# Performance work log

Hardware: AMD Instinct MI355X
Metric: run time of the kernel (lower is better)

The kernel has to match this reference:

```python
import jax, jax.numpy as jnp
import numpy as np

B, S, HID = 2, 2048, 1024
H = 16
D = HID // H  # 64
SCALE = 1.0 / float(np.sqrt(D))


def setup_inputs() -> dict:
    key = jax.random.key(0)
    ks = jax.random.split(key, 12)
    s = 0.02
    return {
        "query": jax.random.normal(ks[0], (B, S, HID), jnp.float32),
        "key": jax.random.normal(ks[1], (B, S, HID), jnp.float32),
        "value": jax.random.normal(ks[2], (B, S, HID), jnp.float32),
        "attention_mask": jnp.ones((B, S, S), jnp.int32),
        "Wq": jax.random.normal(ks[3], (HID, HID), jnp.float32) * s,
        "bq": jnp.zeros((HID,), jnp.float32),
        "Wk": jax.random.normal(ks[4], (HID, HID), jnp.float32) * s,
        "bk": jnp.zeros((HID,), jnp.float32),
        "Wv": jax.random.normal(ks[5], (HID, HID), jnp.float32) * s,
        "bv": jnp.zeros((HID,), jnp.float32),
        "Wo": jax.random.normal(ks[6], (HID, HID), jnp.float32) * s,
        "bo": jnp.zeros((HID,), jnp.float32),
    }


def _split_heads(x):  # [B,S,HID] -> [B,H,S,D]
    b, s, _ = x.shape
    return x.reshape(b, s, H, D).transpose(0, 2, 1, 3)


def reference(query, key, value, attention_mask, Wq, bq, Wk, bk, Wv, bv, Wo, bo):
    # Projections (torch Linear: x @ W.T + b)
    Q = _split_heads(query @ Wq.T + bq)
    K = _split_heads(key @ Wk.T + bk)
    V = _split_heads(value @ Wv.T + bv)
    # Full attention; chunking in the original is math-equivalent (softmax over full key axis per chunk)
    scores = jnp.einsum("bhqd,bhkd->bhqk", Q, K) * SCALE
    scores = jnp.where(attention_mask[:, None, :, :] == 0, jnp.float32(-1e9), scores)
    attn = jax.nn.softmax(scores, axis=-1)  # dropout is identity in eval mode
    ctx = jnp.einsum("bhqk,bhkd->bhqd", attn, V)
    ctx = ctx.transpose(0, 2, 1, 3).reshape(query.shape[0], query.shape[1], HID)
    out = ctx @ Wo.T + bo
    # module returns a dummy uniform attention-weight tensor
    attn_weights = jnp.full((query.shape[0], H, S, S), 1.0 / S, dtype=query.dtype)
    return (out, attn_weights)
```

## Files before the change

kernel.cpp:

```cpp
#include <hip/hip_runtime.h>

typedef float f4v __attribute__((ext_vector_type(4)));
typedef short s4v __attribute__((ext_vector_type(4)));
typedef short s8v __attribute__((ext_vector_type(8)));
typedef __bf16 bf8v __attribute__((ext_vector_type(8)));
typedef unsigned short u16;
typedef unsigned int u32;

#define S_LEN 2048
#define HIDN 1024
#define NH 16
#define HD 64
#define SC2 0.180336879f
#define DTH 11.5415603f
#define FILLV 0.00048828125f

__device__ __forceinline__ u16 f2bf(float f) {
  unsigned u = __builtin_bit_cast(unsigned, f);
  u = u + 0x7FFFu + ((u >> 16) & 1u);
  return (u16)(u >> 16);
}

__device__ __forceinline__ f4v mfma16(s8v a, s8v b, f4v c) {
  return __builtin_amdgcn_mfma_f32_16x16x32_bf16(
      __builtin_bit_cast(bf8v, a), __builtin_bit_cast(bf8v, b), c, 0, 0, 0);
}

__device__ __forceinline__ void gl16(const void* g, void* l) {
  __builtin_amdgcn_global_load_lds((const __attribute__((address_space(1))) u32*)g,
                                   (__attribute__((address_space(3))) u32*)l, 16, 0, 0);
}

__device__ __forceinline__ s8v cvt8(f4v x, f4v y) {
  s8v r;
  r[0] = (short)f2bf(x[0]); r[1] = (short)f2bf(x[1]);
  r[2] = (short)f2bf(x[2]); r[3] = (short)f2bf(x[3]);
  r[4] = (short)f2bf(y[0]); r[5] = (short)f2bf(y[1]);
  r[6] = (short)f2bf(y[2]); r[7] = (short)f2bf(y[3]);
  return r;
}

#define FILL_DECL(nblk)                                        \
  const f4v fvv = (f4v){FILLV, FILLV, FILLV, FILLV};           \
  f4v* fp = fillb + (size_t)bid * 256 + threadIdx.x;           \
  f4v* const fpe = fillb + fill4;                               \
  const size_t FT = (size_t)(nblk) * 256;

#define FILL_STORE()                                           \
  do { if (fp < fpe) __builtin_nontemporal_store(fvv, fp);     \
       fp += FT; } while (0)

struct CvtWArgs { const float* s[4]; u16* d[4]; };

__global__ __launch_bounds__(256) void cvt_w(CvtWArgs a, unsigned* flg) {
  if (blockIdx.x == 0 && blockIdx.y == 0 && threadIdx.x == 0) flg[0] = 1u;
  const float* s = a.s[blockIdx.y];
  u16* d = a.d[blockIdx.y];
  const int stride = gridDim.x * 256;
  for (int i = blockIdx.x * 256 + threadIdx.x; i < 131072; i += stride) {
    const f4v x0 = ((const f4v*)s)[2 * i];
    const f4v x1 = ((const f4v*)s)[2 * i + 1];
    ((s8v*)d)[i] = cvt8(x0, x1);
  }
}

__global__ void pack_mask(const int* __restrict__ mask, unsigned* __restrict__ pmo,
                          unsigned* __restrict__ flg) {
  const size_t total = (size_t)2 * S_LEN * S_LEN;
  size_t i = (size_t)blockIdx.x * blockDim.x + threadIdx.x;
  const size_t st = (size_t)gridDim.x * blockDim.x;
  const int lane = threadIdx.x & 63;
  for (; i < total; i += st) {
    const unsigned long long bb = __ballot(mask[i] != 0);
    if (lane == 0) pmo[i >> 5] = (unsigned)bb;
    if (lane == 32) pmo[i >> 5] = (unsigned)(bb >> 32);
    if (lane == 0 && bb != ~0ull) flg[0] = 0u;
  }
}

struct QkvArgs {
  const float* A[3]; const u16* W[3]; const float* bias[3]; u16* out[3];
  f4v* fillb; size_t fill4;
};

__global__ __launch_bounds__(256) void gemm_qkv(QkvArgs ga) {
  __shared__ __align__(16) u16 As[128 * 32];
  __shared__ __align__(16) u16 Bs[128 * 32];
  const int p = blockIdx.x;
  const int xcd = p & 7;
  const int ii = p >> 3;
  const int ytile = xcd * 12 + (ii >> 3);
  const int xt = ii & 7;
  const int id = ytile >> 5;
  const int tid = threadIdx.x;
  const int lane = tid & 63;
  const int wv = tid >> 6;
  const int wm = wv >> 1, wn = wv & 1;
  const int g = lane >> 4, l15 = lane & 15;
  const int m0 = (ytile & 31) * 128, n0 = xt * 128;
  const int bid = p;
  f4v* fillb = ga.fillb;
  const size_t fill4 = ga.fill4;
  FILL_DECL(768);

  f4v acc[4][4];
#pragma unroll
  for (int i = 0; i < 4; ++i)
#pragma unroll
    for (int j = 0; j < 4; ++j) acc[i][j] = (f4v){0.f, 0.f, 0.f, 0.f};

  const int ar = tid >> 1;
  const int ac = (tid & 1) * 16;
  const float* ap = ga.A[id] + (size_t)(m0 + ar) * HIDN + ac;
  const u16* bp0 = ga.W[id] + (size_t)(n0 + (tid >> 2)) * HIDN + (tid & 3) * 8;
  const u16* bp1 = bp0 + (size_t)64 * HIDN;
  u16* bsl0 = Bs + tid * 8;
  u16* bsl1 = Bs + 2048 + tid * 8;
  u16* asl = As + ar * 32 + ac;

  for (int kt = 0; kt < HIDN; kt += 32) {
    const f4v a0 = ((const f4v*)(ap + kt))[0];
    const f4v a1 = ((const f4v*)(ap + kt))[1];
    const f4v a2 = ((const f4v*)(ap + kt))[2];
    const f4v a3 = ((const f4v*)(ap + kt))[3];
    __syncthreads();
    gl16(bp0 + kt, bsl0);
    gl16(bp1 + kt, bsl1);
    *(s8v*)asl = cvt8(a0, a1);
    *(s8v*)(asl + 8) = cvt8(a2, a3);
    FILL_STORE();
    FILL_STORE();
    __syncthreads();
    s8v af[4], bfv[4];
#pragma unroll
    for (int i = 0; i < 4; ++i)
      af[i] = *(const s8v*)(As + (wm * 64 + i * 16 + l15) * 32 + g * 8);
#pragma unroll
    for (int j = 0; j < 4; ++j)
      bfv[j] = *(const s8v*)(Bs + (wn * 64 + j * 16 + l15) * 32 + g * 8);
#pragma unroll
    for (int i = 0; i < 4; ++i)
#pragma unroll
      for (int j = 0; j < 4; ++j) acc[i][j] = mfma16(af[i], bfv[j], acc[i][j]);
  }

  const float* bias = ga.bias[id];
  u16* out = ga.out[id];
  const int mode2 = (id == 2);
#pragma unroll
  for (int i = 0; i < 4; ++i) {
#pragma unroll
    for (int j = 0; j < 4; ++j) {
      const int mb = m0 + wm * 64 + i * 16 + g * 4;
      const int n = n0 + wn * 64 + j * 16 + l15;
      const float bv = bias[n];
#pragma unroll
      for (int r = 0; r < 4; ++r) {
        const int m = mb + r;
        const float v = acc[i][j][r] + bv;
        const int b = m >> 11, s = m & 2047, h = n >> 6, d = n & 63;
        if (mode2) {
          out[((size_t)(b * NH + h) * HD + d) * S_LEN + s] = f2bf(v);
        } else {
          out[(((size_t)(b * NH + h) * S_LEN + s) << 6) + d] = f2bf(v);
        }
      }
    }
  }
}

__global__ __launch_bounds__(256) void attn_fused(
    const u16* __restrict__ Qb, const u16* __restrict__ Kb,
    const u16* __restrict__ Vtb, u16* __restrict__ ctxb,
    const unsigned* __restrict__ pm, const unsigned* __restrict__ flg,
    f4v* __restrict__ fillb, const size_t fill4) {
  __shared__ __align__(16) u16 Ks[64 * 64];
  __shared__ __align__(16) u16 Vs[64 * 64];
  __shared__ __align__(16) u16 Ps[4][2][16 * 64];
  __shared__ unsigned mw[128][2];

  const int p = blockIdx.x;
  const int xcd = p & 7;
  const int ii = p >> 3;
  const int bh = xcd * 4 + (ii >> 4);
  const int q0 = (ii & 15) * 128;
  const int tid = threadIdx.x;
  const int lane = tid & 63;
  const int wv = tid >> 6;
  const int g = lane >> 4, l15 = lane & 15;
  const int b = bh >> 4, h = bh & 15;
  const bool allones = (flg[0] != 0u);
  const int bid = p;
  FILL_DECL(512);

  s8v qb[2][2];
#pragma unroll
  for (int qg = 0; qg < 2; ++qg) {
    const u16* qp = Qb + ((size_t)bh * S_LEN + q0 + wv * 32 + qg * 16 + l15) * HD + g * 8;
    qb[qg][0] = *(const s8v*)qp;
    qb[qg][1] = *(const s8v*)(qp + 32);
  }

  f4v o[2][4];
#pragma unroll
  for (int qg = 0; qg < 2; ++qg)
#pragma unroll
    for (int nb = 0; nb < 4; ++nb) o[qg][nb] = (f4v){0.f, 0.f, 0.f, 0.f};
  float mr[2] = {-INFINITY, -INFINITY}, lr[2] = {0.f, 0.f};

  const int sr = tid >> 3;
  const int sg = tid & 7;
  const int sc0 = ((sg ^ (sr & 7)) * 8);
  const u16* kp0 = Kb + ((size_t)bh * S_LEN + sr) * HD + sc0;
  const u16* kp1 = kp0 + (size_t)32 * HD;
  const u16* vp0 = Vtb + ((size_t)bh * HD + sr) * S_LEN + sc0;
  const u16* vp1 = vp0 + (size_t)32 * S_LEN;
  u16* kl = Ks + tid * 8;
  u16* vl = Vs + tid * 8;

  for (int kt = 0; kt < S_LEN; kt += 64) {
    __syncthreads();
    gl16(kp0 + (size_t)kt * HD, kl);
    gl16(kp1 + (size_t)kt * HD, kl + 2048);
    gl16(vp0 + kt, vl);
    gl16(vp1 + kt, vl + 2048);
    if (!allones) {
      mw[tid >> 1][tid & 1] =
          pm[((size_t)b * S_LEN + q0 + (tid >> 1)) * (S_LEN / 32) + (kt >> 5) + (tid & 1)];
    }
    FILL_STORE();
    FILL_STORE();
    FILL_STORE();
    FILL_STORE();
    __syncthreads();

    f4v sc[2][4];
    __builtin_amdgcn_s_setprio(1);
#pragma unroll
    for (int nb = 0; nb < 4; ++nb) {
      const int kr = nb * 16 + l15;
      const s8v ka0 = *(const s8v*)(Ks + kr * 64 + ((g ^ (kr & 7)) * 8));
      const s8v ka1 = *(const s8v*)(Ks + kr * 64 + (((4 + g) ^ (kr & 7)) * 8));
#pragma unroll
      for (int qg = 0; qg < 2; ++qg) {
        f4v z = (f4v){0.f, 0.f, 0.f, 0.f};
        z = mfma16(ka0, qb[qg][0], z);
        z = mfma16(ka1, qb[qg][1], z);
        sc[qg][nb] = z * SC2;
      }
    }
    __builtin_amdgcn_s_setprio(0);
    if (!allones) {
#pragma unroll
      for (int qg = 0; qg < 2; ++qg) {
        const int qr = wv * 32 + qg * 16 + l15;
        const unsigned w0 = mw[qr][0], w1 = mw[qr][1];
#pragma unroll
        for (int nb = 0; nb < 4; ++nb) {
          const unsigned wmk = (nb < 2) ? w0 : w1;
#pragma unroll
          for (int r = 0; r < 4; ++r) {
            const int bit = ((nb & 1) << 4) + (g << 2) + r;
            if (!((wmk >> bit) & 1u)) sc[qg][nb][r] = -1e9f;
          }
        }
      }
    }

#pragma unroll
    for (int qg = 0; qg < 2; ++qg) {
      float tm = sc[qg][0][0];
#pragma unroll
      for (int nb = 0; nb < 4; ++nb)
#pragma unroll
        for (int r = 0; r < 4; ++r) tm = fmaxf(tm, sc[qg][nb][r]);
      tm = fmaxf(tm, __shfl_xor(tm, 16, 64));
      tm = fmaxf(tm, __shfl_xor(tm, 32, 64));
      if (!__all(tm <= mr[qg] + DTH)) {
        const float mn = fmaxf(mr[qg], tm);
        const float al = exp2f(mr[qg] - mn);
        mr[qg] = mn;
        lr[qg] *= al;
#pragma unroll
        for (int r = 0; r < 4; ++r) {
          const float ar = __shfl(al, (g << 2) + r, 64);
#pragma unroll
          for (int nb = 0; nb < 4; ++nb) o[qg][nb][r] *= ar;
        }
      }
      float rs = 0.f;
#pragma unroll
      for (int nb = 0; nb < 4; ++nb)
#pragma unroll
        for (int r = 0; r < 4; ++r) {
          const float p_ = exp2f(sc[qg][nb][r] - mr[qg]);
          sc[qg][nb][r] = p_;
          rs += p_;
        }
      rs += __shfl_xor(rs, 16, 64);
      rs += __shfl_xor(rs, 32, 64);
      lr[qg] += rs;
#pragma unroll
      for (int nb = 0; nb < 4; ++nb) {
        s4v pk;
        pk[0] = (short)f2bf(sc[qg][nb][0]);
        pk[1] = (short)f2bf(sc[qg][nb][1]);
        pk[2] = (short)f2bf(sc[qg][nb][2]);
        pk[3] = (short)f2bf(sc[qg][nb][3]);
        *(s4v*)(Ps[wv][qg] + l15 * 64 + ((nb * 16 + g * 4) ^ ((l15 & 7) * 8))) = pk;
      }
    }

    s8v pa[2][2];
#pragma unroll
    for (int qg = 0; qg < 2; ++qg)
#pragma unroll
      for (int kk = 0; kk < 2; ++kk)
        pa[qg][kk] = *(const s8v*)(Ps[wv][qg] + l15 * 64 + (((kk * 4 + g) ^ (l15 & 7)) * 8));

    __builtin_amdgcn_s_setprio(1);
#pragma unroll
    for (int nb = 0; nb < 4; ++nb) {
      const int vr = nb * 16 + l15;
      const s8v vb0 = *(const s8v*)(Vs + vr * 64 + ((g ^ (vr & 7)) * 8));
      const s8v vb1 = *(const s8v*)(Vs + vr * 64 + (((4 + g) ^ (vr & 7)) * 8));
#pragma unroll
      for (int qg = 0; qg < 2; ++qg) {
        o[qg][nb] = mfma16(pa[qg][0], vb0, o[qg][nb]);
        o[qg][nb] = mfma16(pa[qg][1], vb1, o[qg][nb]);
      }
    }
    __builtin_amdgcn_s_setprio(0);
  }

#pragma unroll
  for (int qg = 0; qg < 2; ++qg)
#pragma unroll
    for (int r = 0; r < 4; ++r) {
      const float linv = 1.f / __shfl(lr[qg], (g << 2) + r, 64);
      const int q = q0 + wv * 32 + qg * 16 + g * 4 + r;
#pragma unroll
      for (int nb = 0; nb < 4; ++nb) {
        const int d = nb * 16 + l15;
        ctxb[(((size_t)b * S_LEN + q) * NH + h) * HD + d] = f2bf(o[qg][nb][r] * linv);
      }
    }
}

__global__ __launch_bounds__(256) void gemm_out(
    const u16* __restrict__ A, const u16* __restrict__ W,
    const float* __restrict__ bias, float* __restrict__ out,
    f4v* __restrict__ fillb, const size_t fill4) {
  __shared__ __align__(16) u16 As[128 * 32];
  __shared__ __align__(16) u16 Bs[64 * 32];
  const int p = blockIdx.x;
  const int xcd = p & 7;
  const int ii = p >> 3;
  const int m0 = (xcd * 4 + (ii >> 4)) * 128;
  const int n0 = (ii & 15) * 64;
  const int tid = threadIdx.x;
  const int lane = tid & 63;
  const int wv = tid >> 6;
  const int wm = wv >> 1, wn = wv & 1;
  const int g = lane >> 4, l15 = lane & 15;
  const int bid = p;
  FILL_DECL(512);

  f4v acc[4][2];
#pragma unroll
  for (int i = 0; i < 4; ++i)
#pragma unroll
    for (int j = 0; j < 2; ++j) acc[i][j] = (f4v){0.f, 0.f, 0.f, 0.f};

  const u16* ap0 = A + (size_t)(m0 + (tid >> 2)) * HIDN + (tid & 3) * 8;
  const u16* ap1 = ap0 + (size_t)64 * HIDN;
  const u16* bp0 = W + (size_t)(n0 + (tid >> 2)) * HIDN + (tid & 3) * 8;
  u16* asl0 = As + tid * 8;
  u16* asl1 = As + 2048 + tid * 8;
  u16* bsl0 = Bs + tid * 8;

  for (int kt = 0; kt < HIDN; kt += 32) {
    __syncthreads();
    gl16(ap0 + kt, asl0);
    gl16(ap1 + kt, asl1);
    gl16(bp0 + kt, bsl0);
    FILL_STORE();
    __syncthreads();
    s8v af[4], bfv[2];
#pragma unroll
    for (int i = 0; i < 4; ++i)
      af[i] = *(const s8v*)(As + (wm * 64 + i * 16 + l15) * 32 + g * 8);
#pragma unroll
    for (int j = 0; j < 2; ++j)
      bfv[j] = *(const s8v*)(Bs + (wn * 32 + j * 16 + l15) * 32 + g * 8);
#pragma unroll
    for (int i = 0; i < 4; ++i)
#pragma unroll
      for (int j = 0; j < 2; ++j) acc[i][j] = mfma16(af[i], bfv[j], acc[i][j]);
  }

#pragma unroll
  for (int i = 0; i < 4; ++i) {
#pragma unroll
    for (int j = 0; j < 2; ++j) {
      const int mb = m0 + wm * 64 + i * 16 + g * 4;
      const int n = n0 + wn * 32 + j * 16 + l15;
      const float bv = bias[n];
#pragma unroll
      for (int r = 0; r < 4; ++r) {
        out[(size_t)(mb + r) * HIDN + n] = acc[i][j][r] + bv;
      }
    }
  }
}

__global__ void fill_tail(float* __restrict__ p, const size_t n4) {
  const f4v v = (f4v){FILLV, FILLV, FILLV, FILLV};
  size_t i = (size_t)blockIdx.x * blockDim.x + threadIdx.x;
  const size_t st = (size_t)gridDim.x * blockDim.x;
  f4v* p4 = (f4v*)p;
  for (; i < n4; i += st) p4[i] = v;
}

extern "C" void kernel_launch(void* const* d_in, const int* in_sizes, int n_in,
                              void* d_out, int out_size, void* d_ws, size_t ws_size,
                              hipStream_t stream) {
  const float* query = (const float*)d_in[0];
  const float* key_ = (const float*)d_in[1];
  const float* value = (const float*)d_in[2];
  const int* amask = (const int*)d_in[3];
  const float* Wq = (const float*)d_in[4];
  const float* bq = (const float*)d_in[5];
  const float* Wk = (const float*)d_in[6];
  const float* bk = (const float*)d_in[7];
  const float* Wv = (const float*)d_in[8];
  const float* bv = (const float*)d_in[9];
  const float* Wo = (const float*)d_in[10];
  const float* bo = (const float*)d_in[11];

  float* out = (float*)d_out;
  const size_t OUT0 = (size_t)2 * S_LEN * HIDN;
  float* outw = out + OUT0;

  const size_t MB = (size_t)1 << 20;
  const size_t CARVE = 48 * MB;
  const bool use_ws = ws_size >= CARVE;
  char* scratch = use_ws ? (char*)d_ws : (char*)outw;

  u16* wq16 = (u16*)(scratch);
  u16* wk16 = (u16*)(scratch + 2 * MB);
  u16* wv16 = (u16*)(scratch + 4 * MB);
  u16* wo16 = (u16*)(scratch + 6 * MB);
  u16* Qb = (u16*)(scratch + 8 * MB);
  u16* Kb = (u16*)(scratch + 16 * MB);
  u16* Vtb = (u16*)(scratch + 24 * MB);
  u16* ctxb = (u16*)(scratch + 32 * MB);
  unsigned* pm = (unsigned*)(scratch + 40 * MB);
  unsigned* flg = (unsigned*)(scratch + 41 * MB);

  f4v* fillp;
  size_t F;
  if (use_ws) {
    fillp = (f4v*)outw;
    F = 33554432;
  } else {
    fillp = (f4v*)(outw + CARVE / 4);
    F = 33554432 - CARVE / 16;
  }
  const size_t capq = (size_t)768 * 256 * 64;
  const size_t capa = (size_t)512 * 256 * 128;
  const size_t cq = F < capq ? F : capq;
  const size_t F1 = F - cq;
  const size_t ca = F1 < capa ? F1 : capa;
  const size_t co = F1 - ca;
  f4v* fq = fillp;
  f4v* fa = fq + cq;
  f4v* fo = fa + ca;

  CvtWArgs cw;
  cw.s[0] = Wq; cw.s[1] = Wk; cw.s[2] = Wv; cw.s[3] = Wo;
  cw.d[0] = wq16; cw.d[1] = wk16; cw.d[2] = wv16; cw.d[3] = wo16;
  cvt_w<<<dim3(64, 4), 256, 0, stream>>>(cw, flg);
  pack_mask<<<1024, 256, 0, stream>>>(amask, pm, flg);

  QkvArgs qa;
  qa.A[0] = query; qa.A[1] = key_; qa.A[2] = value;
  qa.W[0] = wq16; qa.W[1] = wk16; qa.W[2] = wv16;
  qa.bias[0] = bq; qa.bias[1] = bk; qa.bias[2] = bv;
  qa.out[0] = Qb; qa.out[1] = Kb; qa.out[2] = Vtb;
  qa.fillb = fq; qa.fill4 = cq;
  gemm_qkv<<<768, 256, 0, stream>>>(qa);

  attn_fused<<<512, 256, 0, stream>>>(Qb, Kb, Vtb, ctxb, pm, flg, fa, ca);

  gemm_out<<<512, 256, 0, stream>>>(ctxb, wo16, bo, out, fo, co);

  if (!use_ws) {
    fill_tail<<<2048, 256, 0, stream>>>(outw, CARVE / 16);
  }
}
```

Before: 203.6 us.

## Halve attention query tile, merge prep kernels, fold Q scale into projection

The attention kernel now handles 64 queries per block (16 per wave) across 1024 blocks instead of 128 per block across 512, which cuts registers and LDS per block and adds parallelism. It also folds the softmax scale into the Q projection epilogue, swaps manual bf16 rounding for native vector conversions, and merges weight conversion and mask packing into one prep kernel with an inverted flag set by memset. Fill stores are moved after the barrier in the GEMMs. The cost is twice as many K/V tile loads from global memory per head and an extra memset launch.

```diff
diff --git a/kernel.cpp b/kernel.cpp
--- a/kernel.cpp
+++ b/kernel.cpp
@@ -1,9 +1,11 @@
 #include <hip/hip_runtime.h>
 
 typedef float f4v __attribute__((ext_vector_type(4)));
+typedef float f8v __attribute__((ext_vector_type(8)));
 typedef short s4v __attribute__((ext_vector_type(4)));
 typedef short s8v __attribute__((ext_vector_type(8)));
-typedef __bf16 bf8v __attribute__((ext_vector_type(8)));
+typedef __bf16 bf4t __attribute__((ext_vector_type(4)));
+typedef __bf16 bf8t __attribute__((ext_vector_type(8)));
 typedef unsigned short u16;
 typedef unsigned int u32;
 
@@ -11,33 +13,31 @@
 #define HIDN 1024
 #define NH 16
 #define HD 64
-#define SC2 0.180336879f
+#define QS 0.180336879f
 #define DTH 11.5415603f
 #define FILLV 0.00048828125f
 
 __device__ __forceinline__ u16 f2bf(float f) {
-  unsigned u = __builtin_bit_cast(unsigned, f);
-  u = u + 0x7FFFu + ((u >> 16) & 1u);
-  return (u16)(u >> 16);
+  return __builtin_bit_cast(u16, (__bf16)f);
+}
+
+__device__ __forceinline__ s8v cvt8(f4v x, f4v y) {
+  const f8v f = {x[0], x[1], x[2], x[3], y[0], y[1], y[2], y[3]};
+  return __builtin_bit_cast(s8v, __builtin_convertvector(f, bf8t));
+}
+
+__device__ __forceinline__ s4v cvt4(f4v x) {
+  return __builtin_bit_cast(s4v, __builtin_convertvector(x, bf4t));
 }
 
 __device__ __forceinline__ f4v mfma16(s8v a, s8v b, f4v c) {
   return __builtin_amdgcn_mfma_f32_16x16x32_bf16(
-      __builtin_bit_cast(bf8v, a), __builtin_bit_cast(bf8v, b), c, 0, 0, 0);
+      __builtin_bit_cast(bf8t, a), __builtin_bit_cast(bf8t, b), c, 0, 0, 0);
 }
 
 __device__ __forceinline__ void gl16(const void* g, void* l) {
   __builtin_amdgcn_global_load_lds((const __attribute__((address_space(1))) u32*)g,
                                    (__attribute__((address_space(3))) u32*)l, 16, 0, 0);
-}
-
-__device__ __forceinline__ s8v cvt8(f4v x, f4v y) {
-  s8v r;
-  r[0] = (short)f2bf(x[0]); r[1] = (short)f2bf(x[1]);
-  r[2] = (short)f2bf(x[2]); r[3] = (short)f2bf(x[3]);
-  r[4] = (short)f2bf(y[0]); r[5] = (short)f2bf(y[1]);
-  r[6] = (short)f2bf(y[2]); r[7] = (short)f2bf(y[3]);
-  return r;
 }
 
 #define FILL_DECL(nblk)                                        \
@@ -50,31 +50,33 @@
   do { if (fp < fpe) __builtin_nontemporal_store(fvv, fp);     \
        fp += FT; } while (0)
 
-struct CvtWArgs { const float* s[4]; u16* d[4]; };
-
-__global__ __launch_bounds__(256) void cvt_w(CvtWArgs a, unsigned* flg) {
-  if (blockIdx.x == 0 && blockIdx.y == 0 && threadIdx.x == 0) flg[0] = 1u;
-  const float* s = a.s[blockIdx.y];
-  u16* d = a.d[blockIdx.y];
-  const int stride = gridDim.x * 256;
-  for (int i = blockIdx.x * 256 + threadIdx.x; i < 131072; i += stride) {
-    const f4v x0 = ((const f4v*)s)[2 * i];
-    const f4v x1 = ((const f4v*)s)[2 * i + 1];
-    ((s8v*)d)[i] = cvt8(x0, x1);
-  }
-}
-
-__global__ void pack_mask(const int* __restrict__ mask, unsigned* __restrict__ pmo,
-                          unsigned* __restrict__ flg) {
-  const size_t total = (size_t)2 * S_LEN * S_LEN;
-  size_t i = (size_t)blockIdx.x * blockDim.x + threadIdx.x;
-  const size_t st = (size_t)gridDim.x * blockDim.x;
-  const int lane = threadIdx.x & 63;
-  for (; i < total; i += st) {
-    const unsigned long long bb = __ballot(mask[i] != 0);
-    if (lane == 0) pmo[i >> 5] = (unsigned)bb;
-    if (lane == 32) pmo[i >> 5] = (unsigned)(bb >> 32);
-    if (lane == 0 && bb != ~0ull) flg[0] = 0u;
+struct PrepArgs { const float* w[4]; u16* d[4]; const int* mask; unsigned* pm; unsigned* flg; };
+
+__global__ __launch_bounds__(256) void prep(PrepArgs a) {
+  const int y = blockIdx.y;
+  const int tid = threadIdx.x;
+  if (y < 4) {
+    const float* s = a.w[y];
+    u16* d = a.d[y];
+#pragma unroll
+    for (int j = 0; j < 2; ++j) {
+      const int i = blockIdx.x * 256 + tid + j * 65536;
+      const f4v x0 = ((const f4v*)s)[2 * i];
+      const f4v x1 = ((const f4v*)s)[2 * i + 1];
+      ((s8v*)d)[i] = cvt8(x0, x1);
+    }
+  } else {
+    const int lane = tid & 63;
+    const size_t base = (size_t)(y - 4) * 2097152;
+    bool anyz = false;
+    for (int j = 0; j < 32; ++j) {
+      const size_t i = base + (size_t)blockIdx.x * 256 + tid + (size_t)j * 65536;
+      const unsigned long long bb = __ballot(a.mask[i] != 0);
+      if (lane == 0) a.pm[i >> 5] = (unsigned)bb;
+      if (lane == 32) a.pm[i >> 5] = (unsigned)(bb >> 32);
+      anyz |= (bb != ~0ull);
+    }
+    if (anyz && lane == 0) a.flg[0] = 1u;
   }
 }
 
@@ -128,9 +130,9 @@
     gl16(bp1 + kt, bsl1);
     *(s8v*)asl = cvt8(a0, a1);
     *(s8v*)(asl + 8) = cvt8(a2, a3);
+    __syncthreads();
     FILL_STORE();
     FILL_STORE();
-    __syncthreads();
     s8v af[4], bfv[4];
 #pragma unroll
     for (int i = 0; i < 4; ++i)
@@ -147,6 +149,7 @@
   const float* bias = ga.bias[id];
   u16* out = ga.out[id];
   const int mode2 = (id == 2);
+  const float osc = (id == 0) ? QS : 1.0f;
 #pragma unroll
   for (int i = 0; i < 4; ++i) {
 #pragma unroll
@@ -157,7 +160,7 @@
 #pragma unroll
       for (int r = 0; r < 4; ++r) {
         const int m = mb + r;
-        const float v = acc[i][j][r] + bv;
+        const float v = (acc[i][j][r] + bv) * osc;
         const int b = m >> 11, s = m & 2047, h = n >> 6, d = n & 63;
         if (mode2) {
           out[((size_t)(b * NH + h) * HD + d) * S_LEN + s] = f2bf(v);
@@ -176,37 +179,31 @@
     f4v* __restrict__ fillb, const size_t fill4) {
   __shared__ __align__(16) u16 Ks[64 * 64];
   __shared__ __align__(16) u16 Vs[64 * 64];
-  __shared__ __align__(16) u16 Ps[4][2][16 * 64];
-  __shared__ unsigned mw[128][2];
+  __shared__ __align__(16) u16 Ps[4][16 * 64];
+  __shared__ unsigned mw[64][2];
 
   const int p = blockIdx.x;
   const int xcd = p & 7;
   const int ii = p >> 3;
-  const int bh = xcd * 4 + (ii >> 4);
-  const int q0 = (ii & 15) * 128;
+  const int bh = xcd * 4 + (ii >> 5);
+  const int q0 = (ii & 31) * 64;
   const int tid = threadIdx.x;
   const int lane = tid & 63;
   const int wv = tid >> 6;
   const int g = lane >> 4, l15 = lane & 15;
   const int b = bh >> 4, h = bh & 15;
-  const bool allones = (flg[0] != 0u);
+  const bool allones = (flg[0] == 0u);
   const int bid = p;
-  FILL_DECL(512);
-
-  s8v qb[2][2];
-#pragma unroll
-  for (int qg = 0; qg < 2; ++qg) {
-    const u16* qp = Qb + ((size_t)bh * S_LEN + q0 + wv * 32 + qg * 16 + l15) * HD + g * 8;
-    qb[qg][0] = *(const s8v*)qp;
-    qb[qg][1] = *(const s8v*)(qp + 32);
-  }
-
-  f4v o[2][4];
-#pragma unroll
-  for (int qg = 0; qg < 2; ++qg)
-#pragma unroll
-    for (int nb = 0; nb < 4; ++nb) o[qg][nb] = (f4v){0.f, 0.f, 0.f, 0.f};
-  float mr[2] = {-INFINITY, -INFINITY}, lr[2] = {0.f, 0.f};
+  FILL_DECL(1024);
+
+  const u16* qp = Qb + ((size_t)bh * S_LEN + q0 + wv * 16 + l15) * HD + g * 8;
+  const s8v qb0 = *(const s8v*)qp;
+  const s8v qb1 = *(const s8v*)(qp + 32);
+
+  f4v o[4];
+#pragma unroll
+  for (int nb = 0; nb < 4; ++nb) o[nb] = (f4v){0.f, 0.f, 0.f, 0.f};
+  float mr = -INFINITY, lr = 0.f;
 
   const int sr = tid >> 3;
   const int sg = tid & 7;
@@ -217,6 +214,7 @@
   const u16* vp1 = vp0 + (size_t)32 * S_LEN;
   u16* kl = Ks + tid * 8;
   u16* vl = Vs + tid * 8;
+  u16* pw = Ps[wv];
 
   for (int kt = 0; kt < S_LEN; kt += 64) {
     __syncthreads();
@@ -224,99 +222,79 @@
     gl16(kp1 + (size_t)kt * HD, kl + 2048);
     gl16(vp0 + kt, vl);
     gl16(vp1 + kt, vl + 2048);
-    if (!allones) {
+    if (!allones && tid < 128) {
       mw[tid >> 1][tid & 1] =
           pm[((size_t)b * S_LEN + q0 + (tid >> 1)) * (S_LEN / 32) + (kt >> 5) + (tid & 1)];
     }
+    __syncthreads();
     FILL_STORE();
     FILL_STORE();
-    FILL_STORE();
-    FILL_STORE();
-    __syncthreads();
-
-    f4v sc[2][4];
+
+    f4v sc[4];
     __builtin_amdgcn_s_setprio(1);
 #pragma unroll
     for (int nb = 0; nb < 4; ++nb) {
       const int kr = nb * 16 + l15;
       const s8v ka0 = *(const s8v*)(Ks + kr * 64 + ((g ^ (kr & 7)) * 8));
       const s8v ka1 = *(const s8v*)(Ks + kr * 64 + (((4 + g) ^ (kr & 7)) * 8));
-#pragma unroll
-      for (int qg = 0; qg < 2; ++qg) {
-        f4v z = (f4v){0.f, 0.f, 0.f, 0.f};
-        z = mfma16(ka0, qb[qg][0], z);
-        z = mfma16(ka1, qb[qg][1], z);
-        sc[qg][nb] = z * SC2;
-      }
+      f4v z = (f4v){0.f, 0.f, 0.f, 0.f};
+      z = mfma16(ka0, qb0, z);
+      z = mfma16(ka1, qb1, z);
+      sc[nb] = z;
     }
     __builtin_amdgcn_s_setprio(0);
     if (!allones) {
-#pragma unroll
-      for (int qg = 0; qg < 2; ++qg) {
-        const int qr = wv * 32 + qg * 16 + l15;
-        const unsigned w0 = mw[qr][0], w1 = mw[qr][1];
-#pragma unroll
-        for (int nb = 0; nb < 4; ++nb) {
-          const unsigned wmk = (nb < 2) ? w0 : w1;
-#pragma unroll
-          for (int r = 0; r < 4; ++r) {
-            const int bit = ((nb & 1) << 4) + (g << 2) + r;
-            if (!((wmk >> bit) & 1u)) sc[qg][nb][r] = -1e9f;
-          }
+      const int qr = wv * 16 + l15;
+      const unsigned w0 = mw[qr][0], w1 = mw[qr][1];
+#pragma unroll
+      for (int nb = 0; nb < 4; ++nb) {
+        const unsigned wmk = (nb < 2) ? w0 : w1;
+#pragma unroll
+        for (int r = 0; r < 4; ++r) {
+          const int bit = ((nb & 1) << 4) + (g << 2) + r;
+          if (!((wmk >> bit) & 1u)) sc[nb][r] = -1e9f;
         }
       }
     }
 
-#pragma unroll
-    for (int qg = 0; qg < 2; ++qg) {
-      float tm = sc[qg][0][0];
-#pragma unroll
-      for (int nb = 0; nb < 4; ++nb)
-#pragma unroll
-        for (int r = 0; r < 4; ++r) tm = fmaxf(tm, sc[qg][nb][r]);
-      tm = fmaxf(tm, __shfl_xor(tm, 16, 64));
-      tm = fmaxf(tm, __shfl_xor(tm, 32, 64));
-      if (!__all(tm <= mr[qg] + DTH)) {
-        const float mn = fmaxf(mr[qg], tm);
-        const float al = exp2f(mr[qg] - mn);
-        mr[qg] = mn;
-        lr[qg] *= al;
-#pragma unroll
-        for (int r = 0; r < 4; ++r) {
-          const float ar = __shfl(al, (g << 2) + r, 64);
-#pragma unroll
-          for (int nb = 0; nb < 4; ++nb) o[qg][nb][r] *= ar;
-        }
+    float tm = sc[0][0];
+#pragma unroll
+    for (int nb = 0; nb < 4; ++nb)
+#pragma unroll
+      for (int r = 0; r < 4; ++r) tm = fmaxf(tm, sc[nb][r]);
+    tm = fmaxf(tm, __shfl_xor(tm, 16, 64));
+    tm = fmaxf(tm, __shfl_xor(tm, 32, 64));
+    if (!__all(tm <= mr + DTH)) {
+      const float mn = fmaxf(mr, tm);
+      const float al = exp2f(mr - mn);
+      mr = mn;
+      lr *= al;
+#pragma unroll
+      for (int r = 0; r < 4; ++r) {
+        const float ar = __shfl(al, (g << 2) + r, 64);
+#pragma unroll
+        for (int nb = 0; nb < 4; ++nb) o[nb][r] *= ar;
       }
-      float rs = 0.f;
-#pragma unroll
-      for (int nb = 0; nb < 4; ++nb)
-#pragma unroll
-        for (int r = 0; r < 4; ++r) {
-          const float p_ = exp2f(sc[qg][nb][r] - mr[qg]);
-          sc[qg][nb][r] = p_;
-          rs += p_;
-        }
-      rs += __shfl_xor(rs, 16, 64);
-      rs += __shfl_xor(rs, 32, 64);
-      lr[qg] += rs;
-#pragma unroll
-      for (int nb = 0; nb < 4; ++nb) {
-        s4v pk;
-        pk[0] = (short)f2bf(sc[qg][nb][0]);
-        pk[1] = (short)f2bf(sc[qg][nb][1]);
-        pk[2] = (short)f2bf(sc[qg][nb][2]);
-        pk[3] = (short)f2bf(sc[qg][nb][3]);
-        *(s4v*)(Ps[wv][qg] + l15 * 64 + ((nb * 16 + g * 4) ^ ((l15 & 7) * 8))) = pk;
+    }
+    float rs = 0.f;
+#pragma unroll
+    for (int nb = 0; nb < 4; ++nb)
+#pragma unroll
+      for (int r = 0; r < 4; ++r) {
+        const float p_ = exp2f(sc[nb][r] - mr);
+        sc[nb][r] = p_;
+        rs += p_;
       }
-    }
-
-    s8v pa[2][2];
-#pragma unroll
-    for (int qg = 0; qg < 2; ++qg)
-#pragma unroll
-      for (int kk = 0; kk < 2; ++kk)
-        pa[qg][kk] = *(const s8v*)(Ps[wv][qg] + l15 * 64 + (((kk * 4 + g) ^ (l15 & 7)) * 8));
+    rs += __shfl_xor(rs, 16, 64);
+    rs += __shfl_xor(rs, 32, 64);
+    lr += rs;
+#pragma unroll
+    for (int nb = 0; nb < 4; ++nb) {
+      *(s4v*)(pw + l15 * 64 + ((nb * 16 + g * 4) ^ ((l15 & 7) * 8))) = cvt4(sc[nb]);
+    }
+
+    const s8v pa0 = *(const s8v*)(pw + l15 * 64 + ((g ^ (l15 & 7)) * 8));
+    const s8v pa1 = *(const s8v*)(pw + l15 * 64 + (((4 + g) ^ (l15 & 7)) * 8));
 
     __builtin_amdgcn_s_setprio(1);
 #pragma unroll
@@ -324,27 +302,22 @@
       const int vr = nb * 16 + l15;
       const s8v vb0 = *(const s8v*)(Vs + vr * 64 + ((g ^ (vr & 7)) * 8));
       const s8v vb1 = *(const s8v*)(Vs + vr * 64 + (((4 + g) ^ (vr & 7)) * 8));
-#pragma unroll
-      for (int qg = 0; qg < 2; ++qg) {
-        o[qg][nb] = mfma16(pa[qg][0], vb0, o[qg][nb]);
-        o[qg][nb] = mfma16(pa[qg][1], vb1, o[qg][nb]);
-      }
+      o[nb] = mfma16(pa0, vb0, o[nb]);
+      o[nb] = mfma16(pa1, vb1, o[nb]);
     }
     __builtin_amdgcn_s_setprio(0);
   }
 
 #pragma unroll
-  for (int qg = 0; qg < 2; ++qg)
-#pragma unroll
-    for (int r = 0; r < 4; ++r) {
-      const float linv = 1.f / __shfl(lr[qg], (g << 2) + r, 64);
-      const int q = q0 + wv * 32 + qg * 16 + g * 4 + r;
-#pragma unroll
-      for (int nb = 0; nb < 4; ++nb) {
-        const int d = nb * 16 + l15;
-        ctxb[(((size_t)b * S_LEN + q) * NH + h) * HD + d] = f2bf(o[qg][nb][r] * linv);
-      }
-    }
+  for (int r = 0; r < 4; ++r) {
+    const float linv = 1.f / __shfl(lr, (g << 2) + r, 64);
+    const int q = q0 + wv * 16 + g * 4 + r;
+#pragma unroll
+    for (int nb = 0; nb < 4; ++nb) {
+      const int d = nb * 16 + l15;
+      ctxb[(((size_t)b * S_LEN + q) * NH + h) * HD + d] = f2bf(o[nb][r] * linv);
+    }
+  }
 }
 
 __global__ __launch_bounds__(256) void gemm_out(
@@ -384,8 +357,8 @@
     gl16(ap0 + kt, asl0);
     gl16(ap1 + kt, asl1);
     gl16(bp0 + kt, bsl0);
+    __syncthreads();
     FILL_STORE();
-    __syncthreads();
     s8v af[4], bfv[2];
 #pragma unroll
     for (int i = 0; i < 4; ++i)
@@ -468,7 +441,7 @@
     F = 33554432 - CARVE / 16;
   }
   const size_t capq = (size_t)768 * 256 * 64;
-  const size_t capa = (size_t)512 * 256 * 128;
+  const size_t capa = (size_t)1024 * 256 * 64;
   const size_t cq = F < capq ? F : capq;
   const size_t F1 = F - cq;
   const size_t ca = F1 < capa ? F1 : capa;
@@ -477,11 +450,13 @@
   f4v* fa = fq + cq;
   f4v* fo = fa + ca;
 
-  CvtWArgs cw;
-  cw.s[0] = Wq; cw.s[1] = Wk; cw.s[2] = Wv; cw.s[3] = Wo;
-  cw.d[0] = wq16; cw.d[1] = wk16; cw.d[2] = wv16; cw.d[3] = wo16;
-  cvt_w<<<dim3(64, 4), 256, 0, stream>>>(cw, flg);
-  pack_mask<<<1024, 256, 0, stream>>>(amask, pm, flg);
+  hipMemsetAsync(flg, 0, 4, stream);
+
+  PrepArgs pa;
+  pa.w[0] = Wq; pa.w[1] = Wk; pa.w[2] = Wv; pa.w[3] = Wo;
+  pa.d[0] = wq16; pa.d[1] = wk16; pa.d[2] = wv16; pa.d[3] = wo16;
+  pa.mask = amask; pa.pm = pm; pa.flg = flg;
+  prep<<<dim3(256, 8), 256, 0, stream>>>(pa);
 
   QkvArgs qa;
   qa.A[0] = query; qa.A[1] = key_; qa.A[2] = value;
@@ -491,7 +466,7 @@
   qa.fillb = fq; qa.fill4 = cq;
   gemm_qkv<<<768, 256, 0, stream>>>(qa);
 
-  attn_fused<<<512, 256, 0, stream>>>(Qb, Kb, Vtb, ctxb, pm, flg, fa, ca);
+  attn_fused<<<1024, 256, 0, stream>>>(Qb, Kb, Vtb, ctxb, pm, flg, fa, ca);
 
   gemm_out<<<512, 256, 0, stream>>>(ctxb, wo16, bo, out, fo, co);
 
```

After: 194.9 us. -4.3%, faster.
